# Kernel tuning notes

Measured on AMD Instinct MI355X. Metric: run time of the kernel, lower is better.

## Reference

```python
import jax, jax.numpy as jnp
import numpy as np

N_HEAD, D_K = 8, 16

def _ln(x, g, b):
    m = jnp.mean(x, -1, keepdims=True)
    v = jnp.var(x, -1, keepdims=True)
    return (x - m) * jax.lax.rsqrt(v + 1e-5) * g + b

def _enc_layer(x, wq, bq, wk, bk, wv, bv, wo, bo, g1, be1, cw1, cb1, cw2, cb2, g2, be2):
    B, L, D = x.shape
    q = (x @ wq + bq).reshape(B, L, N_HEAD, D_K)
    k = (x @ wk + bk).reshape(B, L, N_HEAD, D_K)
    v = (x @ wv + bv).reshape(B, L, N_HEAD, D_K)
    attn = jnp.einsum('blhd,bmhd->bhlm', q, k) / jnp.sqrt(jnp.float32(D_K))
    attn = jax.nn.softmax(attn, axis=-1)
    o = jnp.einsum('bhlm,bmhd->blhd', attn, v).reshape(B, L, -1)
    x = _ln(o @ wo + bo + x, g1, be1)          # post-LN residual (MHA)
    h = jax.nn.relu(x @ cw1 + cb1)             # 1x1 conv == linear
    return _ln(h @ cw2 + cb2 + x, g2, be2)     # post-LN residual (FFN)

def setup_inputs() -> dict:
    key = jax.random.key(0)
    ks = jax.random.split(key, 20)
    N, D, NNZ = 100000, 128, 2000000
    B, L, NL, DI = 32, 256, 2, 512
    s = 0.02
    inp = {}
    inp['ego'] = jax.random.normal(ks[0], (N, D), jnp.float32)
    inp['vals'] = jax.random.uniform(ks[1], (NNZ,), jnp.float32) / 20.0  # ~normalized adj values
    inp['W1'] = jax.random.normal(ks[2], (D, D), jnp.float32) * s
    inp['b1'] = jnp.zeros((D,), jnp.float32)
    inp['W2'] = jax.random.normal(ks[3], (D, D), jnp.float32) * s
    inp['b2'] = jnp.zeros((D,), jnp.float32)
    inp['enc_in'] = jax.random.normal(ks[4], (B, L, D), jnp.float32)
    inp['wq'] = jax.random.normal(ks[5], (NL, D, D), jnp.float32) * s
    inp['bq'] = jnp.zeros((NL, D), jnp.float32)
    inp['wk'] = jax.random.normal(ks[6], (NL, D, D), jnp.float32) * s
    inp['bk'] = jnp.zeros((NL, D), jnp.float32)
    inp['wv'] = jax.random.normal(ks[7], (NL, D, D), jnp.float32) * s
    inp['bv'] = jnp.zeros((NL, D), jnp.float32)
    inp['wo'] = jax.random.normal(ks[8], (NL, D, D), jnp.float32) * s
    inp['bo'] = jnp.zeros((NL, D), jnp.float32)
    inp['ln1_g'] = jnp.ones((NL, D), jnp.float32)
    inp['ln1_b'] = jnp.zeros((NL, D), jnp.float32)
    inp['cw1'] = jax.random.normal(ks[9], (NL, D, DI), jnp.float32) * s
    inp['cb1'] = jnp.zeros((NL, DI), jnp.float32)
    inp['cw2'] = jax.random.normal(ks[10], (NL, DI, D), jnp.float32) * s
    inp['cb2'] = jnp.zeros((NL, D), jnp.float32)
    inp['ln2_g'] = jnp.ones((NL, D), jnp.float32)
    inp['ln2_b'] = jnp.zeros((NL, D), jnp.float32)
    inp['rows'] = jnp.sort(jax.random.randint(ks[11], (NNZ,), 0, N, jnp.int32))
    inp['cols'] = jax.random.randint(ks[12], (NNZ,), 0, N, jnp.int32)
    return inp

def reference(ego, vals, W1, b1, W2, b2, enc_in, wq, bq, wk, bk, wv, bv, wo, bo,
              ln1_g, ln1_b, cw1, cb1, cw2, cb2, ln2_g, ln2_b, rows, cols):
    N = ego.shape[0]
    # sparse A_in @ ego  (COO SpMM via gather + segment_sum)
    side = jax.ops.segment_sum(vals[:, None] * ego[cols], rows, num_segments=N)
    # bi-interaction aggregator (dropout=identity in eval)
    sum_emb = jax.nn.leaky_relu((ego + side) @ W1 + b1)
    bi_emb = jax.nn.leaky_relu((ego * side) @ W2 + b2)
    agg = sum_emb + bi_emb
    # transformer encoder over edge sequences
    x = enc_in
    for i in range(wq.shape[0]):
        x = _enc_layer(x, wq[i], bq[i], wk[i], bk[i], wv[i], bv[i], wo[i], bo[i],
                       ln1_g[i], ln1_b[i], cw1[i], cb1[i], cw2[i], cb2[i], ln2_g[i], ln2_b[i])
    return (agg, x)
```

## Files before the change

kernel.cpp:

```cpp
#include <hip/hip_runtime.h>

typedef __attribute__((ext_vector_type(8))) short bf16x8;
typedef __attribute__((ext_vector_type(4))) float f32x4;

__device__ __forceinline__ unsigned short f2b(float f) {
    union { float f; unsigned int i; } u; u.f = f;
    return (unsigned short)((u.i + 0x7FFFu + ((u.i >> 16) & 1u)) >> 16);
}
__device__ __forceinline__ unsigned int packbf2(float a, float b) {
    return (unsigned int)f2b(a) | ((unsigned int)f2b(b) << 16);
}

__device__ __forceinline__ void spmm_block(
    const unsigned int* __restrict__ egob, const float* __restrict__ vals,
    const int* __restrict__ rows, const int* __restrict__ cols,
    float* __restrict__ side, int nnz, int blk)
{
    int tid = threadIdx.x;
    int wave = tid >> 6, lane = tid & 63;
    int e0 = blk * 256 + wave * 64;
    if (e0 >= nnz) return;

    int idx = e0 + lane;
    int last = nnz - 1;
    bool ok = idx < nnz;
    int safe = ok ? idx : last;
    int my_row = rows[safe];
    int my_col = cols[safe];
    float my_val = ok ? vals[safe] : 0.f;

    int nxt = (e0 + 64 < nnz) ? rows[e0 + 64] : -1;

    unsigned int pre[16];
    #pragma unroll
    for (int j = 0; j < 16; ++j) {
        unsigned int c = (unsigned int)__builtin_amdgcn_readlane(my_col, j);
        pre[j] = *(egob + ((size_t)c << 6) + lane);
    }

    float ax = 0.f, ay = 0.f;
    int cur = __builtin_amdgcn_readlane(my_row, 0);
    bool owned = false;
    #pragma unroll
    for (int e = 0; e < 64; ++e) {
        int r = __builtin_amdgcn_readlane(my_row, e);
        float vv = __int_as_float(__builtin_amdgcn_readlane(__float_as_int(my_val), e));
        unsigned int u = pre[e & 15];
        if (e < 48) {
            unsigned int c = (unsigned int)__builtin_amdgcn_readlane(my_col, e + 16);
            pre[e & 15] = *(egob + ((size_t)c << 6) + lane);
        }
        if (r != cur) {
            if (owned) {
                *(float2*)&side[(size_t)cur * 128 + lane * 2] = make_float2(ax, ay);
            } else {
                atomicAdd(&side[(size_t)cur * 128 + lane * 2], ax);
                atomicAdd(&side[(size_t)cur * 128 + lane * 2 + 1], ay);
            }
            ax = 0.f; ay = 0.f; cur = r; owned = true;
        }
        ax = fmaf(vv, __uint_as_float(u << 16), ax);
        ay = fmaf(vv, __uint_as_float(u & 0xFFFF0000u), ay);
    }
    if (owned && cur != nxt) {
        *(float2*)&side[(size_t)cur * 128 + lane * 2] = make_float2(ax, ay);
    } else {
        atomicAdd(&side[(size_t)cur * 128 + lane * 2], ax);
        atomicAdd(&side[(size_t)cur * 128 + lane * 2 + 1], ay);
    }
}

#define LDAB 40
#define LDBI2 136
#define LDKV 16

__device__ __forceinline__ void gemm2_core(
    const float* __restrict__ A, const float* __restrict__ W,
    const float* __restrict__ bias, const float* __restrict__ R,
    const float* __restrict__ g, const float* __restrict__ bta,
    float* __restrict__ C, int M, int N, int K, int act,
    int bm, int bn, unsigned short* As, unsigned short* Bs,
    float* redS, float* redSS)
{
    int tid = threadIdx.x, wave = tid >> 6, lane = tid & 63;
    int lm = lane & 15, quad = lane >> 4;
    int wm = wave >> 1, wn = wave & 1;

    f32x4 acc[2][4];
    #pragma unroll
    for (int i = 0; i < 2; ++i)
        #pragma unroll
        for (int j = 0; j < 4; ++j) acc[i][j] = (f32x4)(0.f);

    for (int k0 = 0; k0 < K; k0 += 32) {
        {
            int m = tid >> 2, kc = (tid & 3) * 8;
            const float* p = A + (size_t)(bm + m) * K + k0 + kc;
            float4 a0 = *(const float4*)p, a1 = *(const float4*)(p + 4);
            uint4 pk;
            pk.x = packbf2(a0.x, a0.y); pk.y = packbf2(a0.z, a0.w);
            pk.z = packbf2(a1.x, a1.y); pk.w = packbf2(a1.z, a1.w);
            *(uint4*)&As[m * LDAB + kc] = pk;
        }
        {
            int nn = tid & 127, kh = (tid >> 7) * 16;
            const float* p = W + (size_t)(k0 + kh) * N + bn + nn;
            float w[16];
            #pragma unroll
            for (int j = 0; j < 16; ++j) w[j] = p[(size_t)j * N];
            uint4 pk;
            pk.x = packbf2(w[0], w[1]);  pk.y = packbf2(w[2], w[3]);
            pk.z = packbf2(w[4], w[5]);  pk.w = packbf2(w[6], w[7]);
            *(uint4*)&Bs[nn * LDAB + kh] = pk;
            pk.x = packbf2(w[8], w[9]);  pk.y = packbf2(w[10], w[11]);
            pk.z = packbf2(w[12], w[13]); pk.w = packbf2(w[14], w[15]);
            *(uint4*)&Bs[nn * LDAB + kh + 8] = pk;
        }
        __syncthreads();
        bf16x8 af[2], bfr[4];
        #pragma unroll
        for (int mi = 0; mi < 2; ++mi)
            af[mi] = *(bf16x8*)&As[(wm * 32 + mi * 16 + lm) * LDAB + quad * 8];
        #pragma unroll
        for (int ni = 0; ni < 4; ++ni)
            bfr[ni] = *(bf16x8*)&Bs[(wn * 64 + ni * 16 + lm) * LDAB + quad * 8];
        #pragma unroll
        for (int mi = 0; mi < 2; ++mi)
            #pragma unroll
            for (int ni = 0; ni < 4; ++ni)
                acc[mi][ni] = __builtin_amdgcn_mfma_f32_16x16x32_bf16(
                    af[mi], bfr[ni], acc[mi][ni], 0, 0, 0);
        __syncthreads();
    }

    #pragma unroll
    for (int mi = 0; mi < 2; ++mi)
        #pragma unroll
        for (int r = 0; r < 4; ++r) {
            int row = bm + wm * 32 + mi * 16 + quad * 4 + r;
            #pragma unroll
            for (int ni = 0; ni < 4; ++ni) {
                int col = bn + wn * 64 + ni * 16 + lm;
                float v = acc[mi][ni][r] + bias[col];
                if (R) v += R[(size_t)row * N + col];
                if (act) v = fmaxf(v, 0.f);
                C[(size_t)row * N + col] = v;
            }
        }
    (void)g; (void)bta; (void)redS; (void)redSS;
}

__device__ __forceinline__ void gemm3_core(
    const float* __restrict__ A, const unsigned short* __restrict__ Wt,
    const float* __restrict__ bias, const float* __restrict__ R,
    const float* __restrict__ g, const float* __restrict__ bta,
    float* __restrict__ C, int M, int N, int K, int act,
    int bm, int bn, unsigned short* As, float* redS, float* redSS)
{
    int tid = threadIdx.x, wave = tid >> 6, lane = tid & 63;
    int lm = lane & 15, quad = lane >> 4;
    int wm = wave >> 1, wn = wave & 1;

    f32x4 acc[2][4];
    #pragma unroll
    for (int i = 0; i < 2; ++i)
        #pragma unroll
        for (int j = 0; j < 4; ++j) acc[i][j] = (f32x4)(0.f);

    for (int kch = 0; kch < K; kch += 128) {
        if (kch) __syncthreads();
        {
            int m = tid >> 2, kc = (tid & 3) * 32;
            const float* p = A + (size_t)(bm + m) * K + kch + kc;
            float a[32];
            #pragma unroll
            for (int j = 0; j < 8; ++j) {
                float4 av = *(const float4*)(p + j * 4);
                a[j*4+0] = av.x; a[j*4+1] = av.y; a[j*4+2] = av.z; a[j*4+3] = av.w;
            }
            #pragma unroll
            for (int j = 0; j < 4; ++j) {
                int b0 = j * 8;
                uint4 pk;
                pk.x = packbf2(a[b0+0], a[b0+1]); pk.y = packbf2(a[b0+2], a[b0+3]);
                pk.z = packbf2(a[b0+4], a[b0+5]); pk.w = packbf2(a[b0+6], a[b0+7]);
                *(uint4*)&As[m * LDBI2 + kc + b0] = pk;
            }
        }
        __syncthreads();
        #pragma unroll
        for (int ks = 0; ks < 4; ++ks) {
            bf16x8 af[2], bfr[4];
            #pragma unroll
            for (int mi = 0; mi < 2; ++mi)
                af[mi] = *(bf16x8*)&As[(wm * 32 + mi * 16 + lm) * LDBI2 + ks * 32 + quad * 8];
            #pragma unroll
            for (int ni = 0; ni < 4; ++ni) {
                size_t n = (size_t)(bn + wn * 64 + ni * 16 + lm);
                bfr[ni] = *(const bf16x8*)(Wt + n * K + kch + ks * 32 + quad * 8);
            }
            #pragma unroll
            for (int mi = 0; mi < 2; ++mi)
                #pragma unroll
                for (int ni = 0; ni < 4; ++ni)
                    acc[mi][ni] = __builtin_amdgcn_mfma_f32_16x16x32_bf16(
                        af[mi], bfr[ni], acc[mi][ni], 0, 0, 0);
        }
    }

    #pragma unroll
    for (int mi = 0; mi < 2; ++mi)
        #pragma unroll
        for (int r = 0; r < 4; ++r) {
            int row = bm + wm * 32 + mi * 16 + quad * 4 + r;
            #pragma unroll
            for (int ni = 0; ni < 4; ++ni) {
                int col = bn + wn * 64 + ni * 16 + lm;
                float v = acc[mi][ni][r] + bias[col];
                if (R) v += R[(size_t)row * N + col];
                if (act) v = fmaxf(v, 0.f);
                acc[mi][ni][r] = v;
            }
        }

    if (g) {
        #pragma unroll
        for (int mi = 0; mi < 2; ++mi)
            #pragma unroll
            for (int r = 0; r < 4; ++r) {
                float s = 0.f, ss = 0.f;
                #pragma unroll
                for (int ni = 0; ni < 4; ++ni) {
                    float v = acc[mi][ni][r];
                    s += v; ss = fmaf(v, v, ss);
                }
                #pragma unroll
                for (int off = 1; off < 16; off <<= 1) {
                    s  += __shfl_xor(s, off, 64);
                    ss += __shfl_xor(ss, off, 64);
                }
                if (lm == 0) {
                    int lr = wm * 32 + mi * 16 + quad * 4 + r;
                    redS[wn * 64 + lr] = s;
                    redSS[wn * 64 + lr] = ss;
                }
            }
        __syncthreads();
        #pragma unroll
        for (int mi = 0; mi < 2; ++mi)
            #pragma unroll
            for (int r = 0; r < 4; ++r) {
                int lr = wm * 32 + mi * 16 + quad * 4 + r;
                int row = bm + lr;
                float s = redS[lr] + redS[64 + lr];
                float ss = redSS[lr] + redSS[64 + lr];
                float mean = s * (1.f / 128.f);
                float var = ss * (1.f / 128.f) - mean * mean;
                float rstd = rsqrtf(var + 1e-5f);
                #pragma unroll
                for (int ni = 0; ni < 4; ++ni) {
                    int col = wn * 64 + ni * 16 + lm;
                    float y = (acc[mi][ni][r] - mean) * rstd * g[col] + bta[col];
                    C[(size_t)row * 128 + col] = y;
                }
            }
    } else {
        #pragma unroll
        for (int mi = 0; mi < 2; ++mi)
            #pragma unroll
            for (int r = 0; r < 4; ++r) {
                int row = bm + wm * 32 + mi * 16 + quad * 4 + r;
                #pragma unroll
                for (int ni = 0; ni < 4; ++ni) {
                    int col = bn + wn * 64 + ni * 16 + lm;
                    C[(size_t)row * N + col] = acc[mi][ni][r];
                }
            }
    }
}

__device__ __forceinline__ void bi_core4(
    const float* __restrict__ ego, const float* __restrict__ side,
    const unsigned short* __restrict__ W1t, const unsigned short* __restrict__ W2t,
    const float* __restrict__ b1, const float* __restrict__ b2,
    float* __restrict__ out, int M, int bm,
    unsigned short* Us, unsigned short* Ms)
{
    int tid = threadIdx.x, wave = tid >> 6, lane = tid & 63;
    int lm = lane & 15, quad = lane >> 4;
    int wm = wave >> 1, wn = wave & 1;

    f32x4 acc1[2][4], acc2[2][4];
    #pragma unroll
    for (int i = 0; i < 2; ++i)
        #pragma unroll
        for (int j = 0; j < 4; ++j) { acc1[i][j] = (f32x4)(0.f); acc2[i][j] = (f32x4)(0.f); }

    {
        int m = tid >> 2, kc = (tid & 3) * 32;
        int gm = bm + m;
        float e[32], s[32];
        if (gm < M) {
            const float* pe = ego + (size_t)gm * 128 + kc;
            const float* ps = side + (size_t)gm * 128 + kc;
            #pragma unroll
            for (int j = 0; j < 8; ++j) {
                float4 ev = *(const float4*)(pe + j * 4);
                float4 sv = *(const float4*)(ps + j * 4);
                e[j*4+0] = ev.x; e[j*4+1] = ev.y; e[j*4+2] = ev.z; e[j*4+3] = ev.w;
                s[j*4+0] = sv.x; s[j*4+1] = sv.y; s[j*4+2] = sv.z; s[j*4+3] = sv.w;
            }
        } else {
            #pragma unroll
            for (int j = 0; j < 32; ++j) { e[j] = 0.f; s[j] = 0.f; }
        }
        #pragma unroll
        for (int j = 0; j < 4; ++j) {
            int b0 = j * 8;
            uint4 pu, pv;
            pu.x = packbf2(e[b0+0]+s[b0+0], e[b0+1]+s[b0+1]);
            pu.y = packbf2(e[b0+2]+s[b0+2], e[b0+3]+s[b0+3]);
            pu.z = packbf2(e[b0+4]+s[b0+4], e[b0+5]+s[b0+5]);
            pu.w = packbf2(e[b0+6]+s[b0+6], e[b0+7]+s[b0+7]);
            pv.x = packbf2(e[b0+0]*s[b0+0], e[b0+1]*s[b0+1]);
            pv.y = packbf2(e[b0+2]*s[b0+2], e[b0+3]*s[b0+3]);
            pv.z = packbf2(e[b0+4]*s[b0+4], e[b0+5]*s[b0+5]);
            pv.w = packbf2(e[b0+6]*s[b0+6], e[b0+7]*s[b0+7]);
            *(uint4*)&Us[m * LDBI2 + kc + b0] = pu;
            *(uint4*)&Ms[m * LDBI2 + kc + b0] = pv;
        }
    }
    __syncthreads();

    #pragma unroll
    for (int ks = 0; ks < 4; ++ks) {
        bf16x8 au[2], am[2], bf1[4], bf2[4];
        #pragma unroll
        for (int mi = 0; mi < 2; ++mi) {
            int off = (wm * 32 + mi * 16 + lm) * LDBI2 + ks * 32 + quad * 8;
            au[mi] = *(bf16x8*)&Us[off];
            am[mi] = *(bf16x8*)&Ms[off];
        }
        #pragma unroll
        for (int ni = 0; ni < 4; ++ni) {
            size_t n = (size_t)(wn * 64 + ni * 16 + lm);
            size_t koff = n * 128 + ks * 32 + quad * 8;
            bf1[ni] = *(const bf16x8*)(W1t + koff);
            bf2[ni] = *(const bf16x8*)(W2t + koff);
        }
        #pragma unroll
        for (int mi = 0; mi < 2; ++mi)
            #pragma unroll
            for (int ni = 0; ni < 4; ++ni) {
                acc1[mi][ni] = __builtin_amdgcn_mfma_f32_16x16x32_bf16(
                    au[mi], bf1[ni], acc1[mi][ni], 0, 0, 0);
                acc2[mi][ni] = __builtin_amdgcn_mfma_f32_16x16x32_bf16(
                    am[mi], bf2[ni], acc2[mi][ni], 0, 0, 0);
            }
    }
    #pragma unroll
    for (int mi = 0; mi < 2; ++mi)
        #pragma unroll
        for (int r = 0; r < 4; ++r) {
            int row = bm + wm * 32 + mi * 16 + quad * 4 + r;
            if (row < M) {
                #pragma unroll
                for (int ni = 0; ni < 4; ++ni) {
                    int col = wn * 64 + ni * 16 + lm;
                    float v1 = acc1[mi][ni][r] + b1[col];
                    v1 = v1 > 0.f ? v1 : 0.01f * v1;
                    float v2 = acc2[mi][ni][r] + b2[col];
                    v2 = v2 > 0.f ? v2 : 0.01f * v2;
                    out[(size_t)row * 128 + col] = v1 + v2;
                }
            }
        }
}

__device__ __forceinline__ void attn_block(
    const float* __restrict__ q, const float* __restrict__ k,
    const float* __restrict__ v, float* __restrict__ o, int NH,
    int blk, float* Ks, float* Vs)
{
    const int L = 256, DK = 16;
    int bh = blk >> 2, qq = blk & 3;
    int b = bh / NH, h = bh % NH;
    int tid = threadIdx.x;
    int qi = tid >> 2, seg = tid & 3;

    int lq = qq * 64 + qi;
    size_t qbase = ((size_t)(b * L + lq) * NH + h) * DK;
    float qr[16];
    #pragma unroll
    for (int d4 = 0; d4 < 4; ++d4) {
        float4 t = *(const float4*)(q + qbase + d4 * 4);
        qr[d4*4+0] = t.x * 0.25f; qr[d4*4+1] = t.y * 0.25f;
        qr[d4*4+2] = t.z * 0.25f; qr[d4*4+3] = t.w * 0.25f;
    }
    float acc[16];
    #pragma unroll
    for (int d = 0; d < 16; ++d) acc[d] = 0.f;
    float mmax = -1e30f, ssum = 0.f;

    for (int c0 = 0; c0 < L; c0 += 128) {
        __syncthreads();
        for (int i = tid; i < 128 * 4; i += 256) {
            int ll = i >> 2, d4 = (i & 3) * 4;
            size_t gg = ((size_t)(b * L + c0 + ll) * NH + h) * DK + d4;
            *(float4*)&Ks[ll * LDKV + d4] = *(const float4*)(k + gg);
            *(float4*)&Vs[ll * LDKV + d4] = *(const float4*)(v + gg);
        }
        __syncthreads();

        for (int i = 0; i < 32; ++i) {
            int kk = (i << 2) | seg;
            const float* kr = &Ks[kk * LDKV];
            float dot = 0.f;
            #pragma unroll
            for (int d4 = 0; d4 < 4; ++d4) {
                float4 kv = *(const float4*)&kr[d4 * 4];
                dot = fmaf(qr[d4*4+0], kv.x, dot);
                dot = fmaf(qr[d4*4+1], kv.y, dot);
                dot = fmaf(qr[d4*4+2], kv.z, dot);
                dot = fmaf(qr[d4*4+3], kv.w, dot);
            }
            if (dot > mmax) {
                float alpha = __expf(mmax - dot);
                ssum *= alpha;
                #pragma unroll
                for (int d = 0; d < 16; ++d) acc[d] *= alpha;
                mmax = dot;
            }
            float p = __expf(dot - mmax);
            ssum += p;
            const float* vr = &Vs[kk * LDKV];
            #pragma unroll
            for (int d4 = 0; d4 < 4; ++d4) {
                float4 vv = *(const float4*)&vr[d4 * 4];
                acc[d4*4+0] = fmaf(p, vv.x, acc[d4*4+0]);
                acc[d4*4+1] = fmaf(p, vv.y, acc[d4*4+1]);
                acc[d4*4+2] = fmaf(p, vv.z, acc[d4*4+2]);
                acc[d4*4+3] = fmaf(p, vv.w, acc[d4*4+3]);
            }
        }
    }

    float m1 = fmaxf(mmax, __shfl_xor(mmax, 1, 64));
    float m2 = fmaxf(m1, __shfl_xor(m1, 2, 64));
    float f = __expf(mmax - m2);
    float sl = ssum * f;
    sl += __shfl_xor(sl, 1, 64);
    sl += __shfl_xor(sl, 2, 64);
    #pragma unroll
    for (int d = 0; d < 16; ++d) {
        float a = acc[d] * f;
        a += __shfl_xor(a, 1, 64);
        a += __shfl_xor(a, 2, 64);
        acc[d] = a;
    }
    if (seg == 0) {
        float inv = 1.f / sl;
        #pragma unroll
        for (int d4 = 0; d4 < 4; ++d4) {
            float4 t;
            t.x = acc[d4*4+0] * inv; t.y = acc[d4*4+1] * inv;
            t.z = acc[d4*4+2] * inv; t.w = acc[d4*4+3] * inv;
            *(float4*)(o + qbase + d4 * 4) = t;
        }
    }
}


__global__ __launch_bounds__(256) void qkv2_pre(
    const float* __restrict__ A,
    const float* __restrict__ wq, const float* __restrict__ wk, const float* __restrict__ wv,
    const float* __restrict__ bq, const float* __restrict__ bk, const float* __restrict__ bv,
    float* __restrict__ Q, float* __restrict__ Ko, float* __restrict__ V, int M, int encGy,
    float* __restrict__ side, int Nn,
    const float* __restrict__ ego, unsigned int* __restrict__ egob,
    const float* __restrict__ W1, const float* __restrict__ W2,
    unsigned short* __restrict__ W1t, unsigned short* __restrict__ W2t,
    const float* __restrict__ cw1, const float* __restrict__ cw2,
    const float* __restrict__ wo,
    unsigned short* __restrict__ wt, int NL,
    int encN, int ZB, int CB, int WTB, int EWB)
{
    __shared__ unsigned short As[64 * LDAB];
    __shared__ unsigned short Bs[128 * LDAB];
    __shared__ float redS[128], redSS[128];
    int gid = blockIdx.x;
    int tid = threadIdx.x;
    if (gid >= encN) {
        int j = gid - encN;
        if (j < ZB) {
            size_t n4 = (size_t)Nn * 32;
            float4 z = make_float4(0.f, 0.f, 0.f, 0.f);
            for (size_t i = (size_t)j * 256 + tid; i < n4; i += (size_t)ZB * 256)
                ((float4*)side)[i] = z;
        } else if (j < ZB + CB) {
            int c = j - ZB;
            size_t n4 = (size_t)Nn * 32;
            for (size_t i = (size_t)c * 256 + tid; i < n4; i += (size_t)CB * 256) {
                float4 a = *(const float4*)(ego + i * 4);
                uint2 p;
                p.x = packbf2(a.x, a.y);
                p.y = packbf2(a.z, a.w);
                *(uint2*)(egob + i * 2) = p;
            }
        } else if (j < ZB + CB + WTB) {
            int c = j - ZB - CB;
            for (int ch = c * 256 + tid; ch < 4096; ch += WTB * 256) {
                int w = ch >> 11, rem = ch & 2047;
                int n = rem >> 4, k8 = rem & 15;
                const float* src = w ? W2 : W1;
                unsigned short* dst = w ? W2t : W1t;
                float t[8];
                #pragma unroll
                for (int jj = 0; jj < 8; ++jj)
                    t[jj] = src[(size_t)(k8 * 8 + jj) * 128 + n];
                uint4 pk;
                pk.x = packbf2(t[0], t[1]); pk.y = packbf2(t[2], t[3]);
                pk.z = packbf2(t[4], t[5]); pk.w = packbf2(t[6], t[7]);
                *(uint4*)&dst[(size_t)n * 128 + k8 * 8] = pk;
            }
        } else {
            int c = j - ZB - CB - WTB;
            int total = NL * 24576;
            for (int u = c * 256 + tid; u < total; u += EWB * 256) {
                int layer = u / 24576, w = u % 24576;
                const float* src; unsigned short* dst; int K, N, n, k8;
                if (w < 8192) {
                    int mi = w >> 11, r = w & 2047;
                    src = (mi == 0 ? wq : mi == 1 ? wk : mi == 2 ? wv : wo)
                          + (size_t)layer * 16384;
                    dst = wt + (size_t)layer * 196608 + mi * 16384;
                    K = 128; N = 128; n = r >> 4; k8 = r & 15;
                } else if (w < 16384) {
                    int r = w - 8192;
                    src = cw1 + (size_t)layer * 65536;
                    dst = wt + (size_t)layer * 196608 + 65536;
                    K = 128; N = 512; n = r >> 4; k8 = r & 15;
                } else {
                    int r = w - 16384;
                    src = cw2 + (size_t)layer * 65536;
                    dst = wt + (size_t)layer * 196608 + 131072;
                    K = 512; N = 128; n = r >> 6; k8 = r & 63;
                }
                float t[8];
                #pragma unroll
                for (int jj = 0; jj < 8; ++jj)
                    t[jj] = src[(size_t)(k8 * 8 + jj) * N + n];
                uint4 pk;
                pk.x = packbf2(t[0], t[1]); pk.y = packbf2(t[2], t[3]);
                pk.z = packbf2(t[4], t[5]); pk.w = packbf2(t[6], t[7]);
                *(uint4*)&dst[(size_t)n * K + k8 * 8] = pk;
            }
        }
        return;
    }
    int sel = gid / encGy, by = gid % encGy;
    const float* W = (sel == 0) ? wq : (sel == 1) ? wk : wv;
    const float* b = (sel == 0) ? bq : (sel == 1) ? bk : bv;
    float* C = (sel == 0) ? Q : (sel == 1) ? Ko : V;
    gemm2_core(A, W, b, nullptr, nullptr, nullptr, C, M, 128, 128, 0,
               by * 64, 0, As, Bs, redS, redSS);
}

__global__ __launch_bounds__(256) void qkv3_spmm(
    const float* __restrict__ A, const unsigned short* __restrict__ wtL,
    const float* __restrict__ bq, const float* __restrict__ bk, const float* __restrict__ bv,
    float* __restrict__ Q, float* __restrict__ Ko, float* __restrict__ V, int M, int encGy,
    const unsigned int* __restrict__ egob, const float* __restrict__ vals,
    const int* __restrict__ rows, const int* __restrict__ cols,
    float* __restrict__ side, int nnz, int spmmBase, int encN)
{
    __shared__ unsigned short As[64 * LDBI2];
    __shared__ float redS[128], redSS[128];
    int gid = blockIdx.x;
    if (gid >= encN) {
        spmm_block(egob, vals, rows, cols, side, nnz, spmmBase + gid - encN);
        return;
    }
    int sel = gid / encGy, by = gid % encGy;
    const unsigned short* Wt = wtL + sel * 16384;
    const float* b = (sel == 0) ? bq : (sel == 1) ? bk : bv;
    float* C = (sel == 0) ? Q : (sel == 1) ? Ko : V;
    gemm3_core(A, Wt, b, nullptr, nullptr, nullptr, C, M, 128, 128, 0,
               by * 64, 0, As, redS, redSS);
}

__global__ __launch_bounds__(256) void gemm3_spmm(
    const float* __restrict__ A, const unsigned short* __restrict__ Wt,
    const float* __restrict__ bias, const float* __restrict__ R,
    const float* __restrict__ g, const float* __restrict__ bta,
    float* __restrict__ C, int M, int N, int K, int act, int encGy,
    const unsigned int* __restrict__ egob, const float* __restrict__ vals,
    const int* __restrict__ rows, const int* __restrict__ cols,
    float* __restrict__ side, int nnz, int spmmBase, int encN)
{
    __shared__ unsigned short As[64 * LDBI2];
    __shared__ float redS[128], redSS[128];
    int gid = blockIdx.x;
    if (gid >= encN) {
        spmm_block(egob, vals, rows, cols, side, nnz, spmmBase + gid - encN);
        return;
    }
    int bx = gid / encGy, by = gid % encGy;
    gemm3_core(A, Wt, bias, R, g, bta, C, M, N, K, act,
               by * 64, bx * 128, As, redS, redSS);
}

__global__ __launch_bounds__(256) void gemm3_bi4(
    const float* __restrict__ A, const unsigned short* __restrict__ Wt,
    const float* __restrict__ bias, const float* __restrict__ R,
    const float* __restrict__ g, const float* __restrict__ bta,
    float* __restrict__ C, int M, int N, int K, int act, int encGy,
    const float* __restrict__ ego, const float* __restrict__ side,
    const unsigned short* __restrict__ W1t, const unsigned short* __restrict__ W2t,
    const float* __restrict__ b1, const float* __restrict__ b2,
    float* __restrict__ out, int Mbi, int biBase, int biCnt)
{
    __shared__ uint4 smem4[34816 / 16];
    char* smem = (char*)smem4;
    int gid = blockIdx.x;
    if (gid < biCnt) {
        int bb = biBase + gid;
        unsigned short* Us = (unsigned short*)smem;
        unsigned short* Ms = (unsigned short*)(smem + 17408);
        bi_core4(ego, side, W1t, W2t, b1, b2, out, Mbi, bb * 64, Us, Ms);
    } else {
        int egid = gid - biCnt;
        unsigned short* As = (unsigned short*)smem;
        float* redS  = (float*)(smem + 17408);
        float* redSS = (float*)(smem + 17408 + 512);
        int bx = egid / encGy, by = egid % encGy;
        gemm3_core(A, Wt, bias, R, g, bta, C, M, N, K, act,
                   by * 64, bx * 128, As, redS, redSS);
    }
}

__global__ __launch_bounds__(256) void attn_spmm(
    const float* __restrict__ q, const float* __restrict__ k,
    const float* __restrict__ v, float* __restrict__ o, int NH,
    const unsigned int* __restrict__ egob, const float* __restrict__ vals,
    const int* __restrict__ rows, const int* __restrict__ cols,
    float* __restrict__ side, int nnz, int spmmBase, int encN)
{
    __shared__ float Ks[128 * LDKV];
    __shared__ float Vs[128 * LDKV];
    int gid = blockIdx.x;
    if (gid >= encN) {
        spmm_block(egob, vals, rows, cols, side, nnz, spmmBase + gid - encN);
        return;
    }
    attn_block(q, k, v, o, NH, gid, Ks, Vs);
}

extern "C" void kernel_launch(void* const* d_in, const int* in_sizes, int n_in,
                              void* d_out, int out_size, void* d_ws, size_t ws_size,
                              hipStream_t stream) {
    const float* ego    = (const float*)d_in[0];
    const float* vals   = (const float*)d_in[1];
    const float* W1     = (const float*)d_in[2];
    const float* b1     = (const float*)d_in[3];
    const float* W2     = (const float*)d_in[4];
    const float* b2     = (const float*)d_in[5];
    const float* enc_in = (const float*)d_in[6];
    const float* wq  = (const float*)d_in[7];
    const float* bq  = (const float*)d_in[8];
    const float* wk  = (const float*)d_in[9];
    const float* bk  = (const float*)d_in[10];
    const float* wv  = (const float*)d_in[11];
    const float* bv  = (const float*)d_in[12];
    const float* wo  = (const float*)d_in[13];
    const float* bo  = (const float*)d_in[14];
    const float* ln1_g = (const float*)d_in[15];
    const float* ln1_b = (const float*)d_in[16];
    const float* cw1 = (const float*)d_in[17];
    const float* cb1 = (const float*)d_in[18];
    const float* cw2 = (const float*)d_in[19];
    const float* cb2 = (const float*)d_in[20];
    const float* ln2_g = (const float*)d_in[21];
    const float* ln2_b = (const float*)d_in[22];
    const int* rows = (const int*)d_in[23];
    const int* cols = (const int*)d_in[24];

    const int D = 128, DI = 512, NH = 8, L = 256;
    const int Nn   = in_sizes[0] / D;
    const int nnz  = in_sizes[1];
    const int NL   = in_sizes[7] / (D * D);
    const int Menc = in_sizes[6] / D;
    const int Bb   = Menc / L;

    float* ws = (float*)d_ws;
    size_t off = 0;
    float* side = ws + off; off += (size_t)Nn * D;
    float* Qb = ws + off; off += (size_t)Menc * D;
    float* Kb = ws + off; off += (size_t)Menc * D;
    float* Vb = ws + off; off += (size_t)Menc * D;
    float* Ob = ws + off; off += (size_t)Menc * D;
    float* XA = ws + off; off += (size_t)Menc * D;
    float* XB = ws + off; off += (size_t)Menc * D;
    float* Hb = ws + off; off += (size_t)Menc * DI;
    unsigned int* egob = (unsigned int*)(ws + off); off += (size_t)Nn * (D / 2);
    unsigned short* W1t = (unsigned short*)(ws + off); off += (size_t)D * D / 2;
    unsigned short* W2t = (unsigned short*)(ws + off); off += (size_t)D * D / 2;
    unsigned short* wt  = (unsigned short*)(ws + off); off += (size_t)NL * 196608 / 2;

    float* outAgg = (float*)d_out;
    float* outX   = (float*)d_out + (size_t)Nn * D;

    const int spmmBlocks = (nnz + 255) / 256;
    const int nSpmmStages = 5 * NL - 3;
    const int perS = (spmmBlocks + nSpmmStages - 1) / nSpmmStages;
    const int biTiles = (Nn + 63) / 64;
    const int perB = (biTiles + 1) / 2;
    const int biStart = 5 * NL - 1;
    const int encGy = Menc / 64;
    const int ZB = 512, CB = 1024, WTB = 16, EWB = 64;
    int sidx = 0, sci = 0, bci = 0;

    const float* x = enc_in;
    for (int i = 0; i < NL; ++i) {
        const size_t wOff = (size_t)i * D * D;
        const unsigned short* wtL = wt + (size_t)i * 196608;
        int base, cnt;
        #define SPMM_CHUNK base = sci * perS; cnt = spmmBlocks - base; \
                           if (cnt < 0) cnt = 0; if (cnt > perS) cnt = perS; sci++
        #define BI_CHUNK   base = bci * perB; cnt = biTiles - base; \
                           if (cnt < 0) cnt = 0; if (cnt > perB) cnt = perB; bci++

        sidx++;
        if (sidx == 1) {
            qkv2_pre<<<3 * encGy + ZB + CB + WTB + EWB, 256, 0, stream>>>(
                x, wq + wOff, wk + wOff, wv + wOff,
                bq + (size_t)i * D, bk + (size_t)i * D, bv + (size_t)i * D,
                Qb, Kb, Vb, Menc, encGy,
                side, Nn, ego, egob, W1, W2, W1t, W2t,
                cw1, cw2, wo, wt, NL, 3 * encGy, ZB, CB, WTB, EWB);
        } else {
            SPMM_CHUNK;
            qkv3_spmm<<<3 * encGy + cnt, 256, 0, stream>>>(
                x, wtL,
                bq + (size_t)i * D, bk + (size_t)i * D, bv + (size_t)i * D,
                Qb, Kb, Vb, Menc, encGy,
                egob, vals, rows, cols, side, nnz, base, 3 * encGy);
        }

        sidx++;
        SPMM_CHUNK;
        attn_spmm<<<Bb * NH * 4 + cnt, 256, 0, stream>>>(
            Qb, Kb, Vb, Ob, NH,
            egob, vals, rows, cols, side, nnz, base, Bb * NH * 4);

        sidx++;
        SPMM_CHUNK;
        gemm3_spmm<<<encGy + cnt, 256, 0, stream>>>(
            Ob, wtL + 49152, bo + (size_t)i * D, x,
            ln1_g + (size_t)i * D, ln1_b + (size_t)i * D, XA, Menc, D, D, 0, encGy,
            egob, vals, rows, cols, side, nnz, base, encGy);

        sidx++;
        if (sidx >= biStart) {
            BI_CHUNK;
            gemm3_bi4<<<4 * encGy + cnt, 256, 0, stream>>>(
                XA, wtL + 65536, cb1 + (size_t)i * DI, nullptr,
                nullptr, nullptr, Hb, Menc, DI, D, 1, encGy,
                ego, side, W1t, W2t, b1, b2, outAgg, Nn, base, cnt);
        } else {
            SPMM_CHUNK;
            gemm3_spmm<<<4 * encGy + cnt, 256, 0, stream>>>(
                XA, wtL + 65536, cb1 + (size_t)i * DI, nullptr,
                nullptr, nullptr, Hb, Menc, DI, D, 1, encGy,
                egob, vals, rows, cols, side, nnz, base, 4 * encGy);
        }

        sidx++;
        float* dst = (i == NL - 1) ? outX : XB;
        if (sidx >= biStart) {
            BI_CHUNK;
            gemm3_bi4<<<encGy + cnt, 256, 0, stream>>>(
                Hb, wtL + 131072, cb2 + (size_t)i * D, XA,
                ln2_g + (size_t)i * D, ln2_b + (size_t)i * D, dst, Menc, D, DI, 0, encGy,
                ego, side, W1t, W2t, b1, b2, outAgg, Nn, base, cnt);
        } else {
            SPMM_CHUNK;
            gemm3_spmm<<<encGy + cnt, 256, 0, stream>>>(
                Hb, wtL + 131072, cb2 + (size_t)i * D, XA,
                ln2_g + (size_t)i * D, ln2_b + (size_t)i * D, dst, Menc, D, DI, 0, encGy,
                egob, vals, rows, cols, side, nnz, base, encGy);
        }
        #undef SPMM_CHUNK
        #undef BI_CHUNK
        x = XB;
    }
}
```

Before: 439.7 us.

## Front-load SpMM into first two stages and spread bi-interaction across remaining launches

Weight/ego preprocessing moves into a standalone pre-kernel launched before the encoder, and the first-layer QKV projection now uses the pre-transposed bf16 weights. The SpMM work, previously spread over most encoder stages, is split into two halves co-scheduled with the first QKV and attention launches. Bi-interaction tiles are then spread across all later stages, including a new fused QKV+bi kernel. This aims to finish the scatter-atomics early and balance side work better against encoder kernels. The cost is an extra serialized launch, and heavier SpMM load in the first two stages.

```diff
diff --git a/kernel.cpp b/kernel.cpp
--- a/kernel.cpp
+++ b/kernel.cpp
@@ -70,85 +70,8 @@
     }
 }
 
-#define LDAB 40
 #define LDBI2 136
 #define LDKV 16
-
-__device__ __forceinline__ void gemm2_core(
-    const float* __restrict__ A, const float* __restrict__ W,
-    const float* __restrict__ bias, const float* __restrict__ R,
-    const float* __restrict__ g, const float* __restrict__ bta,
-    float* __restrict__ C, int M, int N, int K, int act,
-    int bm, int bn, unsigned short* As, unsigned short* Bs,
-    float* redS, float* redSS)
-{
-    int tid = threadIdx.x, wave = tid >> 6, lane = tid & 63;
-    int lm = lane & 15, quad = lane >> 4;
-    int wm = wave >> 1, wn = wave & 1;
-
-    f32x4 acc[2][4];
-    #pragma unroll
-    for (int i = 0; i < 2; ++i)
-        #pragma unroll
-        for (int j = 0; j < 4; ++j) acc[i][j] = (f32x4)(0.f);
-
-    for (int k0 = 0; k0 < K; k0 += 32) {
-        {
-            int m = tid >> 2, kc = (tid & 3) * 8;
-            const float* p = A + (size_t)(bm + m) * K + k0 + kc;
-            float4 a0 = *(const float4*)p, a1 = *(const float4*)(p + 4);
-            uint4 pk;
-            pk.x = packbf2(a0.x, a0.y); pk.y = packbf2(a0.z, a0.w);
-            pk.z = packbf2(a1.x, a1.y); pk.w = packbf2(a1.z, a1.w);
-            *(uint4*)&As[m * LDAB + kc] = pk;
-        }
-        {
-            int nn = tid & 127, kh = (tid >> 7) * 16;
-            const float* p = W + (size_t)(k0 + kh) * N + bn + nn;
-            float w[16];
-            #pragma unroll
-            for (int j = 0; j < 16; ++j) w[j] = p[(size_t)j * N];
-            uint4 pk;
-            pk.x = packbf2(w[0], w[1]);  pk.y = packbf2(w[2], w[3]);
-            pk.z = packbf2(w[4], w[5]);  pk.w = packbf2(w[6], w[7]);
-            *(uint4*)&Bs[nn * LDAB + kh] = pk;
-            pk.x = packbf2(w[8], w[9]);  pk.y = packbf2(w[10], w[11]);
-            pk.z = packbf2(w[12], w[13]); pk.w = packbf2(w[14], w[15]);
-            *(uint4*)&Bs[nn * LDAB + kh + 8] = pk;
-        }
-        __syncthreads();
-        bf16x8 af[2], bfr[4];
-        #pragma unroll
-        for (int mi = 0; mi < 2; ++mi)
-            af[mi] = *(bf16x8*)&As[(wm * 32 + mi * 16 + lm) * LDAB + quad * 8];
-        #pragma unroll
-        for (int ni = 0; ni < 4; ++ni)
-            bfr[ni] = *(bf16x8*)&Bs[(wn * 64 + ni * 16 + lm) * LDAB + quad * 8];
-        #pragma unroll
-        for (int mi = 0; mi < 2; ++mi)
-            #pragma unroll
-            for (int ni = 0; ni < 4; ++ni)
-                acc[mi][ni] = __builtin_amdgcn_mfma_f32_16x16x32_bf16(
-                    af[mi], bfr[ni], acc[mi][ni], 0, 0, 0);
-        __syncthreads();
-    }
-
-    #pragma unroll
-    for (int mi = 0; mi < 2; ++mi)
-        #pragma unroll
-        for (int r = 0; r < 4; ++r) {
-            int row = bm + wm * 32 + mi * 16 + quad * 4 + r;
-            #pragma unroll
-            for (int ni = 0; ni < 4; ++ni) {
-                int col = bn + wn * 64 + ni * 16 + lm;
-                float v = acc[mi][ni][r] + bias[col];
-                if (R) v += R[(size_t)row * N + col];
-                if (act) v = fmaxf(v, 0.f);
-                C[(size_t)row * N + col] = v;
-            }
-        }
-    (void)g; (void)bta; (void)redS; (void)redSS;
-}
 
 __device__ __forceinline__ void gemm3_core(
     const float* __restrict__ A, const unsigned short* __restrict__ Wt,
@@ -471,99 +394,83 @@
 }
 
 
-__global__ __launch_bounds__(256) void qkv2_pre(
-    const float* __restrict__ A,
-    const float* __restrict__ wq, const float* __restrict__ wk, const float* __restrict__ wv,
-    const float* __restrict__ bq, const float* __restrict__ bk, const float* __restrict__ bv,
-    float* __restrict__ Q, float* __restrict__ Ko, float* __restrict__ V, int M, int encGy,
+__global__ __launch_bounds__(256) void pre_kernel(
     float* __restrict__ side, int Nn,
     const float* __restrict__ ego, unsigned int* __restrict__ egob,
     const float* __restrict__ W1, const float* __restrict__ W2,
     unsigned short* __restrict__ W1t, unsigned short* __restrict__ W2t,
+    const float* __restrict__ wq, const float* __restrict__ wk,
+    const float* __restrict__ wv, const float* __restrict__ wo,
     const float* __restrict__ cw1, const float* __restrict__ cw2,
-    const float* __restrict__ wo,
     unsigned short* __restrict__ wt, int NL,
-    int encN, int ZB, int CB, int WTB, int EWB)
-{
-    __shared__ unsigned short As[64 * LDAB];
-    __shared__ unsigned short Bs[128 * LDAB];
-    __shared__ float redS[128], redSS[128];
-    int gid = blockIdx.x;
+    int ZB, int CB, int WTB, int EWB)
+{
+    int j = blockIdx.x;
     int tid = threadIdx.x;
-    if (gid >= encN) {
-        int j = gid - encN;
-        if (j < ZB) {
-            size_t n4 = (size_t)Nn * 32;
-            float4 z = make_float4(0.f, 0.f, 0.f, 0.f);
-            for (size_t i = (size_t)j * 256 + tid; i < n4; i += (size_t)ZB * 256)
-                ((float4*)side)[i] = z;
-        } else if (j < ZB + CB) {
-            int c = j - ZB;
-            size_t n4 = (size_t)Nn * 32;
-            for (size_t i = (size_t)c * 256 + tid; i < n4; i += (size_t)CB * 256) {
-                float4 a = *(const float4*)(ego + i * 4);
-                uint2 p;
-                p.x = packbf2(a.x, a.y);
-                p.y = packbf2(a.z, a.w);
-                *(uint2*)(egob + i * 2) = p;
-            }
-        } else if (j < ZB + CB + WTB) {
-            int c = j - ZB - CB;
-            for (int ch = c * 256 + tid; ch < 4096; ch += WTB * 256) {
-                int w = ch >> 11, rem = ch & 2047;
-                int n = rem >> 4, k8 = rem & 15;
-                const float* src = w ? W2 : W1;
-                unsigned short* dst = w ? W2t : W1t;
-                float t[8];
-                #pragma unroll
-                for (int jj = 0; jj < 8; ++jj)
-                    t[jj] = src[(size_t)(k8 * 8 + jj) * 128 + n];
-                uint4 pk;
-                pk.x = packbf2(t[0], t[1]); pk.y = packbf2(t[2], t[3]);
-                pk.z = packbf2(t[4], t[5]); pk.w = packbf2(t[6], t[7]);
-                *(uint4*)&dst[(size_t)n * 128 + k8 * 8] = pk;
-            }
-        } else {
-            int c = j - ZB - CB - WTB;
-            int total = NL * 24576;
-            for (int u = c * 256 + tid; u < total; u += EWB * 256) {
-                int layer = u / 24576, w = u % 24576;
-                const float* src; unsigned short* dst; int K, N, n, k8;
-                if (w < 8192) {
-                    int mi = w >> 11, r = w & 2047;
-                    src = (mi == 0 ? wq : mi == 1 ? wk : mi == 2 ? wv : wo)
-                          + (size_t)layer * 16384;
-                    dst = wt + (size_t)layer * 196608 + mi * 16384;
-                    K = 128; N = 128; n = r >> 4; k8 = r & 15;
-                } else if (w < 16384) {
-                    int r = w - 8192;
-                    src = cw1 + (size_t)layer * 65536;
-                    dst = wt + (size_t)layer * 196608 + 65536;
-                    K = 128; N = 512; n = r >> 4; k8 = r & 15;
-                } else {
-                    int r = w - 16384;
-                    src = cw2 + (size_t)layer * 65536;
-                    dst = wt + (size_t)layer * 196608 + 131072;
-                    K = 512; N = 128; n = r >> 6; k8 = r & 63;
-                }
-                float t[8];
-                #pragma unroll
-                for (int jj = 0; jj < 8; ++jj)
-                    t[jj] = src[(size_t)(k8 * 8 + jj) * N + n];
-                uint4 pk;
-                pk.x = packbf2(t[0], t[1]); pk.y = packbf2(t[2], t[3]);
-                pk.z = packbf2(t[4], t[5]); pk.w = packbf2(t[6], t[7]);
-                *(uint4*)&dst[(size_t)n * K + k8 * 8] = pk;
-            }
-        }
-        return;
-    }
-    int sel = gid / encGy, by = gid % encGy;
-    const float* W = (sel == 0) ? wq : (sel == 1) ? wk : wv;
-    const float* b = (sel == 0) ? bq : (sel == 1) ? bk : bv;
-    float* C = (sel == 0) ? Q : (sel == 1) ? Ko : V;
-    gemm2_core(A, W, b, nullptr, nullptr, nullptr, C, M, 128, 128, 0,
-               by * 64, 0, As, Bs, redS, redSS);
+    if (j < ZB) {
+        size_t n4 = (size_t)Nn * 32;
+        float4 z = make_float4(0.f, 0.f, 0.f, 0.f);
+        for (size_t i = (size_t)j * 256 + tid; i < n4; i += (size_t)ZB * 256)
+            ((float4*)side)[i] = z;
+    } else if (j < ZB + CB) {
+        int c = j - ZB;
+        size_t n4 = (size_t)Nn * 32;
+        for (size_t i = (size_t)c * 256 + tid; i < n4; i += (size_t)CB * 256) {
+            float4 a = *(const float4*)(ego + i * 4);
+            uint2 p;
+            p.x = packbf2(a.x, a.y);
+            p.y = packbf2(a.z, a.w);
+            *(uint2*)(egob + i * 2) = p;
+        }
+    } else if (j < ZB + CB + WTB) {
+        int c = j - ZB - CB;
+        for (int ch = c * 256 + tid; ch < 4096; ch += WTB * 256) {
+            int w = ch >> 11, rem = ch & 2047;
+            int n = rem >> 4, k8 = rem & 15;
+            const float* src = w ? W2 : W1;
+            unsigned short* dst = w ? W2t : W1t;
+            float t[8];
+            #pragma unroll
+            for (int jj = 0; jj < 8; ++jj)
+                t[jj] = src[(size_t)(k8 * 8 + jj) * 128 + n];
+            uint4 pk;
+            pk.x = packbf2(t[0], t[1]); pk.y = packbf2(t[2], t[3]);
+            pk.z = packbf2(t[4], t[5]); pk.w = packbf2(t[6], t[7]);
+            *(uint4*)&dst[(size_t)n * 128 + k8 * 8] = pk;
+        }
+    } else {
+        int c = j - ZB - CB - WTB;
+        int total = NL * 24576;
+        for (int u = c * 256 + tid; u < total; u += EWB * 256) {
+            int layer = u / 24576, w = u % 24576;
+            const float* src; unsigned short* dst; int K, N, n, k8;
+            if (w < 8192) {
+                int mi = w >> 11, r = w & 2047;
+                src = (mi == 0 ? wq : mi == 1 ? wk : mi == 2 ? wv : wo)
+                      + (size_t)layer * 16384;
+                dst = wt + (size_t)layer * 196608 + mi * 16384;
+                K = 128; N = 128; n = r >> 4; k8 = r & 15;
+            } else if (w < 16384) {
+                int r = w - 8192;
+                src = cw1 + (size_t)layer * 65536;
+                dst = wt + (size_t)layer * 196608 + 65536;
+                K = 128; N = 512; n = r >> 4; k8 = r & 15;
+            } else {
+                int r = w - 16384;
+                src = cw2 + (size_t)layer * 65536;
+                dst = wt + (size_t)layer * 196608 + 131072;
+                K = 512; N = 128; n = r >> 6; k8 = r & 63;
+            }
+            float t[8];
+            #pragma unroll
+            for (int jj = 0; jj < 8; ++jj)
+                t[jj] = src[(size_t)(k8 * 8 + jj) * N + n];
+            uint4 pk;
+            pk.x = packbf2(t[0], t[1]); pk.y = packbf2(t[2], t[3]);
+            pk.z = packbf2(t[4], t[5]); pk.w = packbf2(t[6], t[7]);
+            *(uint4*)&dst[(size_t)n * K + k8 * 8] = pk;
+        }
+    }
 }
 
 __global__ __launch_bounds__(256) void qkv3_spmm(
@@ -589,25 +496,35 @@
                by * 64, 0, As, redS, redSS);
 }
 
-__global__ __launch_bounds__(256) void gemm3_spmm(
-    const float* __restrict__ A, const unsigned short* __restrict__ Wt,
-    const float* __restrict__ bias, const float* __restrict__ R,
-    const float* __restrict__ g, const float* __restrict__ bta,
-    float* __restrict__ C, int M, int N, int K, int act, int encGy,
-    const unsigned int* __restrict__ egob, const float* __restrict__ vals,
-    const int* __restrict__ rows, const int* __restrict__ cols,
-    float* __restrict__ side, int nnz, int spmmBase, int encN)
-{
-    __shared__ unsigned short As[64 * LDBI2];
-    __shared__ float redS[128], redSS[128];
+__global__ __launch_bounds__(256) void qkv3_bi(
+    const float* __restrict__ A, const unsigned short* __restrict__ wtL,
+    const float* __restrict__ bq, const float* __restrict__ bk, const float* __restrict__ bv,
+    float* __restrict__ Q, float* __restrict__ Ko, float* __restrict__ V, int M, int encGy,
+    const float* __restrict__ ego, const float* __restrict__ side,
+    const unsigned short* __restrict__ W1t, const unsigned short* __restrict__ W2t,
+    const float* __restrict__ b1, const float* __restrict__ b2,
+    float* __restrict__ out, int Mbi, int biBase, int biCnt)
+{
+    __shared__ uint4 smem4[34816 / 16];
+    char* smem = (char*)smem4;
     int gid = blockIdx.x;
-    if (gid >= encN) {
-        spmm_block(egob, vals, rows, cols, side, nnz, spmmBase + gid - encN);
+    if (gid < biCnt) {
+        int bb = biBase + gid;
+        unsigned short* Us = (unsigned short*)smem;
+        unsigned short* Ms = (unsigned short*)(smem + 17408);
+        bi_core4(ego, side, W1t, W2t, b1, b2, out, Mbi, bb * 64, Us, Ms);
         return;
     }
-    int bx = gid / encGy, by = gid % encGy;
-    gemm3_core(A, Wt, bias, R, g, bta, C, M, N, K, act,
-               by * 64, bx * 128, As, redS, redSS);
+    int egid = gid - biCnt;
+    unsigned short* As = (unsigned short*)smem;
+    float* redS  = (float*)(smem + 17408);
+    float* redSS = (float*)(smem + 17408 + 512);
+    int sel = egid / encGy, by = egid % encGy;
+    const unsigned short* Wt = wtL + sel * 16384;
+    const float* b = (sel == 0) ? bq : (sel == 1) ? bk : bv;
+    float* C = (sel == 0) ? Q : (sel == 1) ? Ko : V;
+    gemm3_core(A, Wt, b, nullptr, nullptr, nullptr, C, M, 128, 128, 0,
+               by * 64, 0, As, redS, redSS);
 }
 
 __global__ __launch_bounds__(256) void gemm3_bi4(
@@ -711,86 +628,66 @@
     float* outX   = (float*)d_out + (size_t)Nn * D;
 
     const int spmmBlocks = (nnz + 255) / 256;
-    const int nSpmmStages = 5 * NL - 3;
-    const int perS = (spmmBlocks + nSpmmStages - 1) / nSpmmStages;
+    const int spmmHalf = (spmmBlocks + 1) / 2;
     const int biTiles = (Nn + 63) / 64;
-    const int perB = (biTiles + 1) / 2;
-    const int biStart = 5 * NL - 1;
+    const int nBiStages = 5 * NL - 3;
+    const int perB = (biTiles + nBiStages - 1) / nBiStages;
     const int encGy = Menc / 64;
     const int ZB = 512, CB = 1024, WTB = 16, EWB = 64;
-    int sidx = 0, sci = 0, bci = 0;
+    int bci = 0;
+
+    pre_kernel<<<ZB + CB + WTB + EWB, 256, 0, stream>>>(
+        side, Nn, ego, egob, W1, W2, W1t, W2t,
+        wq, wk, wv, wo, cw1, cw2, wt, NL, ZB, CB, WTB, EWB);
 
     const float* x = enc_in;
     for (int i = 0; i < NL; ++i) {
-        const size_t wOff = (size_t)i * D * D;
         const unsigned short* wtL = wt + (size_t)i * 196608;
         int base, cnt;
-        #define SPMM_CHUNK base = sci * perS; cnt = spmmBlocks - base; \
-                           if (cnt < 0) cnt = 0; if (cnt > perS) cnt = perS; sci++
-        #define BI_CHUNK   base = bci * perB; cnt = biTiles - base; \
-                           if (cnt < 0) cnt = 0; if (cnt > perB) cnt = perB; bci++
-
-        sidx++;
-        if (sidx == 1) {
-            qkv2_pre<<<3 * encGy + ZB + CB + WTB + EWB, 256, 0, stream>>>(
-                x, wq + wOff, wk + wOff, wv + wOff,
-                bq + (size_t)i * D, bk + (size_t)i * D, bv + (size_t)i * D,
+        #define BI_CHUNK base = bci * perB; cnt = biTiles - base; \
+                         if (cnt < 0) cnt = 0; if (cnt > perB) cnt = perB; bci++
+
+        if (i == 0) {
+            qkv3_spmm<<<3 * encGy + spmmHalf, 256, 0, stream>>>(
+                x, wtL, bq + (size_t)i * D, bk + (size_t)i * D, bv + (size_t)i * D,
                 Qb, Kb, Vb, Menc, encGy,
-                side, Nn, ego, egob, W1, W2, W1t, W2t,
-                cw1, cw2, wo, wt, NL, 3 * encGy, ZB, CB, WTB, EWB);
+                egob, vals, rows, cols, side, nnz, 0, 3 * encGy);
         } else {
-            SPMM_CHUNK;
-            qkv3_spmm<<<3 * encGy + cnt, 256, 0, stream>>>(
-                x, wtL,
-                bq + (size_t)i * D, bk + (size_t)i * D, bv + (size_t)i * D,
+            BI_CHUNK;
+            qkv3_bi<<<3 * encGy + cnt, 256, 0, stream>>>(
+                x, wtL, bq + (size_t)i * D, bk + (size_t)i * D, bv + (size_t)i * D,
                 Qb, Kb, Vb, Menc, encGy,
-                egob, vals, rows, cols, side, nnz, base, 3 * encGy);
-        }
-
-        sidx++;
-        SPMM_CHUNK;
-        attn_spmm<<<Bb * NH * 4 + cnt, 256, 0, stream>>>(
-            Qb, Kb, Vb, Ob, NH,
-            egob, vals, rows, cols, side, nnz, base, Bb * NH * 4);
-
-        sidx++;
-        SPMM_CHUNK;
-        gemm3_spmm<<<encGy + cnt, 256, 0, stream>>>(
+                ego, side, W1t, W2t, b1, b2, outAgg, Nn, base, cnt);
+        }
+
+        if (i == 0) {
+            attn_spmm<<<Bb * NH * 4 + (spmmBlocks - spmmHalf), 256, 0, stream>>>(
+                Qb, Kb, Vb, Ob, NH,
+                egob, vals, rows, cols, side, nnz, spmmHalf, Bb * NH * 4);
+        } else {
+            attn_spmm<<<Bb * NH * 4, 256, 0, stream>>>(
+                Qb, Kb, Vb, Ob, NH,
+                egob, vals, rows, cols, side, nnz, 0, Bb * NH * 4);
+        }
+
+        BI_CHUNK;
+        gemm3_bi4<<<encGy + cnt, 256, 0, stream>>>(
             Ob, wtL + 49152, bo + (size_t)i * D, x,
             ln1_g + (size_t)i * D, ln1_b + (size_t)i * D, XA, Menc, D, D, 0, encGy,
-            egob, vals, rows, cols, side, nnz, base, encGy);
-
-        sidx++;
-        if (sidx >= biStart) {
-            BI_CHUNK;
-            gemm3_bi4<<<4 * encGy + cnt, 256, 0, stream>>>(
-                XA, wtL + 65536, cb1 + (size_t)i * DI, nullptr,
-                nullptr, nullptr, Hb, Menc, DI, D, 1, encGy,
-                ego, side, W1t, W2t, b1, b2, outAgg, Nn, base, cnt);
-        } else {
-            SPMM_CHUNK;
-            gemm3_spmm<<<4 * encGy + cnt, 256, 0, stream>>>(
-                XA, wtL + 65536, cb1 + (size_t)i * DI, nullptr,
-                nullptr, nullptr, Hb, Menc, DI, D, 1, encGy,
-                egob, vals, rows, cols, side, nnz, base, 4 * encGy);
-        }
-
-        sidx++;
+            ego, side, W1t, W2t, b1, b2, outAgg, Nn, base, cnt);
+
+        BI_CHUNK;
+        gemm3_bi4<<<4 * encGy + cnt, 256, 0, stream>>>(
+            XA, wtL + 65536, cb1 + (size_t)i * DI, nullptr,
+            nullptr, nullptr, Hb, Menc, DI, D, 1, encGy,
+            ego, side, W1t, W2t, b1, b2, outAgg, Nn, base, cnt);
+
+        BI_CHUNK;
         float* dst = (i == NL - 1) ? outX : XB;
-        if (sidx >= biStart) {
-            BI_CHUNK;
-            gemm3_bi4<<<encGy + cnt, 256, 0, stream>>>(
-                Hb, wtL + 131072, cb2 + (size_t)i * D, XA,
-                ln2_g + (size_t)i * D, ln2_b + (size_t)i * D, dst, Menc, D, DI, 0, encGy,
-                ego, side, W1t, W2t, b1, b2, outAgg, Nn, base, cnt);
-        } else {
-            SPMM_CHUNK;
-            gemm3_spmm<<<encGy + cnt, 256, 0, stream>>>(
-                Hb, wtL + 131072, cb2 + (size_t)i * D, XA,
-                ln2_g + (size_t)i * D, ln2_b + (size_t)i * D, dst, Menc, D, DI, 0, encGy,
-                egob, vals, rows, cols, side, nnz, base, encGy);
-        }
-        #undef SPMM_CHUNK
+        gemm3_bi4<<<encGy + cnt, 256, 0, stream>>>(
+            Hb, wtL + 131072, cb2 + (size_t)i * D, XA,
+            ln2_g + (size_t)i * D, ln2_b + (size_t)i * D, dst, Menc, D, DI, 0, encGy,
+            ego, side, W1t, W2t, b1, b2, outAgg, Nn, base, cnt);
         #undef BI_CHUNK
         x = XB;
     }
```

After: 458.0 us. 4.2% more time.
